# Kernel tuning notes

Measured on AMD Instinct MI355X. Metric: run time of the kernel, lower is better.

Reference implementation:

```python
import jax, jax.numpy as jnp
import numpy as np

B, S, D, H = 4, 2048, 1024, 16
DEPTH = D // H
NEG = 1e10


def setup_inputs() -> dict:
    key = jax.random.key(0)
    ks = jax.random.split(key, 11)
    sc = 0.02
    return {
        "q": jax.random.normal(ks[0], (B, S, D), jnp.float32),
        "v": jax.random.normal(ks[1], (B, S, D), jnp.float32),
        "k": jax.random.normal(ks[2], (B, S, D), jnp.float32),
        "Wq": jax.random.normal(ks[3], (D, D), jnp.float32) * sc,
        "bq": jnp.zeros((D,), jnp.float32),
        "Wk": jax.random.normal(ks[4], (D, D), jnp.float32) * sc,
        "bk": jnp.zeros((D,), jnp.float32),
        "Wv": jax.random.normal(ks[5], (D, D), jnp.float32) * sc,
        "bv": jnp.zeros((D,), jnp.float32),
        "Wo": jax.random.normal(ks[6], (D, D), jnp.float32) * sc,
        "bo": jnp.zeros((D,), jnp.float32),
        "mask": 1,
    }


def _split_heads(x):
    # [B, S, D] -> [B, H, S, depth]
    b, s, _ = x.shape
    return x.reshape(b, s, H, DEPTH).transpose(0, 2, 1, 3)


def reference(q, v, k, Wq, bq, Wk, bk, Wv, bv, Wo, bo, mask):
    qh = _split_heads(q @ Wq + bq)
    kh = _split_heads(k @ Wk + bk)
    vh = _split_heads(v @ Wv + bv)

    scale = 1.0 / jnp.sqrt(jnp.asarray(DEPTH, jnp.float32))
    # [B, H, Sq, Sk]
    logits = jnp.einsum("bhqd,bhkd->bhqk", qh, kh) * scale

    if mask:
        nd, ns = logits.shape[-2], logits.shape[-1]
        i = jnp.arange(nd)[:, None]
        j = jnp.arange(ns)[None, :]
        b = (i >= j - ns + nd).astype(logits.dtype)  # lower triangle from lower-right
        logits = logits * b - NEG * (1.0 - b)

    attn = jax.nn.softmax(logits, axis=-1)
    out = jnp.einsum("bhqk,bhkd->bhqd", attn, vh)  # [B, H, Sq, depth]
    out = out.transpose(0, 2, 1, 3).reshape(q.shape[0], -1, D)  # concat heads
    return out @ Wo + bo
```

## Files before the change

kernel.cpp:

```cpp
#include <hip/hip_runtime.h>
#include <hip/hip_bf16.h>
#include <cstdint>
#include <cstddef>

#define S_LEN 2048
#define D_MODEL 1024
#define N_HEADS 16
#define DEPTH 64
#define BATCH 4

typedef __attribute__((ext_vector_type(4))) float f32x4;
typedef __attribute__((ext_vector_type(8))) short bf16x8;
typedef __attribute__((ext_vector_type(4))) unsigned short us4;
typedef __attribute__((ext_vector_type(8))) unsigned short us8;

__device__ __forceinline__ unsigned short f2bf(float f) {
  unsigned int u = __builtin_bit_cast(unsigned int, f);
  u += 0x7FFFu + ((u >> 16) & 1u);
  return (unsigned short)(u >> 16);
}

__device__ __forceinline__ unsigned short f2bf_hw(float f) {
  return __builtin_bit_cast(unsigned short, __float2bfloat16(f));
}

struct TCArgs {
  const float* W[4];
  unsigned short* Wt[4];
  float scale[4];
};

__global__ __launch_bounds__(256) void transpose_cast4(TCArgs a, int N) {
  __shared__ float tile[32][33];
  int z = blockIdx.z;
  const float* W = a.W[z];
  unsigned short* Wt = a.Wt[z];
  float scale = a.scale[z];
  int bx = blockIdx.x * 32;
  int by = blockIdx.y * 32;
  int tx = threadIdx.x, ty = threadIdx.y;
#pragma unroll
  for (int i = 0; i < 4; ++i)
    tile[ty + i * 8][tx] = W[(size_t)(by + ty + i * 8) * N + bx + tx];
  __syncthreads();
#pragma unroll
  for (int i = 0; i < 4; ++i)
    Wt[(size_t)(bx + ty + i * 8) * N + by + tx] = f2bf(tile[tx][ty + i * 8] * scale);
}

__global__ __launch_bounds__(256) void transpose_v(const unsigned short* __restrict__ Vp,
                                                   unsigned short* __restrict__ Vt) {
  __shared__ unsigned short tile[64][72];
  int tid = threadIdx.x;
  int sb = blockIdx.x;
  int bh = blockIdx.y;
  int b = bh >> 4, h = bh & 15;
  int s0 = sb * 64;
#pragma unroll
  for (int rep = 0; rep < 2; ++rep) {
    int idx = rep * 256 + tid;
    int r = idx >> 3, c8 = idx & 7;
    us8 v = *(const us8*)(Vp + (size_t)(b * S_LEN + s0 + r) * D_MODEL + h * DEPTH + c8 * 8);
#pragma unroll
    for (int e = 0; e < 8; ++e) tile[c8 * 8 + e][r] = v[e];
  }
  __syncthreads();
#pragma unroll
  for (int rep = 0; rep < 2; ++rep) {
    int idx = rep * 256 + tid;
    int d = idx >> 3, c8 = idx & 7;
    us8 v = *(const us8*)&tile[d][c8 * 8];
    *(us8*)(Vt + ((size_t)(bh * DEPTH + d)) * S_LEN + s0 + c8 * 8) = v;
  }
}

struct GemmSlice {
  const void* A;
  const unsigned short* Bt;
  const float* bias;
  void* C;
  float bscale;
};
struct GemmArgs {
  GemmSlice s[3];
};

template <bool A_IS_F32, bool OUT_F32>
__global__ __launch_bounds__(256) void gemm_bt(GemmArgs args, int M, int N, int K) {
  constexpr int ASTR = A_IS_F32 ? 72 : 76;
  constexpr int BSTR = 76;
  __shared__ unsigned short a_lds[128 * ASTR];
  __shared__ unsigned short b_lds[128 * BSTR];

  int slice = blockIdx.y >> 3;
  int nj = blockIdx.y & 7;
  const GemmSlice& g = args.s[slice];
  const float* Af = (const float*)g.A;
  const unsigned short* Ah = (const unsigned short*)g.A;
  const unsigned short* Bt = g.Bt;

  int tid = threadIdx.x;
  int wave = tid >> 6, lane = tid & 63;
  int l15 = lane & 15, lg = lane >> 4;
  int wm = wave >> 1, wn = wave & 1;

  int row0 = blockIdx.x * 128;
  int col0 = nj * 128;

  f32x4 acc[4][4] = {};
  f32x4 av[8];
  us8 avh[4];
  us8 bv[4];

  int ar = tid >> 4, ac4 = tid & 15;
  int br = tid >> 3, bc8 = tid & 7;

  auto loadA = [&](int k0) {
#pragma unroll
    for (int rep = 0; rep < 8; ++rep)
      av[rep] = *(const f32x4*)(Af + (size_t)(row0 + rep * 16 + ar) * K + k0 + ac4 * 4);
  };
  auto writeA = [&]() {
#pragma unroll
    for (int rep = 0; rep < 8; ++rep) {
      us4 h = {f2bf_hw(av[rep][0]), f2bf_hw(av[rep][1]),
               f2bf_hw(av[rep][2]), f2bf_hw(av[rep][3])};
      *(us4*)&a_lds[(rep * 16 + ar) * 72 + ac4 * 4] = h;
    }
  };
  auto loadAh = [&](int k0) {
#pragma unroll
    for (int rep = 0; rep < 4; ++rep)
      avh[rep] = *(const us8*)(Ah + (size_t)(row0 + rep * 32 + br) * K + k0 + bc8 * 8);
  };
  auto writeAh = [&]() {
#pragma unroll
    for (int rep = 0; rep < 4; ++rep)
      *(us8*)&a_lds[(rep * 32 + br) * 76 + bc8 * 8] = avh[rep];
  };
  auto loadB = [&](int k0) {
#pragma unroll
    for (int rep = 0; rep < 4; ++rep)
      bv[rep] = *(const us8*)(Bt + (size_t)(col0 + rep * 32 + br) * K + k0 + bc8 * 8);
  };
  auto writeB = [&]() {
#pragma unroll
    for (int rep = 0; rep < 4; ++rep)
      *(us8*)&b_lds[(rep * 32 + br) * BSTR + bc8 * 8] = bv[rep];
  };
  auto compute = [&]() {
#pragma unroll
    for (int kk = 0; kk < 2; ++kk) {
      bf16x8 af[4], bfr[4];
#pragma unroll
      for (int ii = 0; ii < 4; ++ii) {
        int row = wm * 64 + ii * 16 + l15;
        af[ii] = *(const bf16x8*)&a_lds[row * ASTR + kk * 32 + lg * 8];
      }
#pragma unroll
      for (int jj = 0; jj < 4; ++jj) {
        int row = wn * 64 + jj * 16 + l15;
        bfr[jj] = *(const bf16x8*)&b_lds[row * BSTR + kk * 32 + lg * 8];
      }
#pragma unroll
      for (int ii = 0; ii < 4; ++ii)
#pragma unroll
        for (int jj = 0; jj < 4; ++jj)
          acc[ii][jj] = __builtin_amdgcn_mfma_f32_16x16x32_bf16(af[ii], bfr[jj], acc[ii][jj], 0, 0, 0);
    }
  };

  int nk = K >> 6;
  loadB(0);
  if constexpr (A_IS_F32) loadA(0); else loadAh(0);

  for (int ki = 0; ki < nk; ++ki) {
    __syncthreads();
    writeB();
    if constexpr (A_IS_F32) writeA(); else writeAh();
    __syncthreads();
    if (ki + 1 < nk) {
      loadB((ki + 1) * 64);
      if constexpr (A_IS_F32) loadA((ki + 1) * 64); else loadAh((ki + 1) * 64);
    }
    compute();
  }

#pragma unroll
  for (int ii = 0; ii < 4; ++ii) {
#pragma unroll
    for (int jj = 0; jj < 4; ++jj) {
      int col = col0 + wn * 64 + jj * 16 + l15;
      float bv2 = g.bias[col] * g.bscale;
#pragma unroll
      for (int r = 0; r < 4; ++r) {
        int row = row0 + wm * 64 + ii * 16 + lg * 4 + r;
        float v = acc[ii][jj][r] + bv2;
        if constexpr (OUT_F32)
          ((float*)g.C)[(size_t)row * N + col] = v;
        else
          ((unsigned short*)g.C)[(size_t)row * N + col] = f2bf(v);
      }
    }
  }
}

__global__ __launch_bounds__(256) void attn_kernel(const unsigned short* __restrict__ Qp,
                                                   const unsigned short* __restrict__ Kp,
                                                   const unsigned short* __restrict__ Vt,
                                                   unsigned short* __restrict__ Op) {
  __shared__ unsigned short k_lds[64][76];
  __shared__ unsigned short vt_lds[64][76];
  __shared__ unsigned short p_lds[4][32][76];

  int tid = threadIdx.x;
  int w = tid >> 6, lane = tid & 63;
  int l15 = lane & 15, lg = lane >> 4;

  int bid = blockIdx.x;
  int swz = (bid & 7) * 64 + (bid >> 3);
  int pairIdx = swz & 7;
  int bh = swz >> 3;
  int b = bh >> 4, h = bh & 15;

  const unsigned short* Kbase = Kp + (size_t)b * S_LEN * D_MODEL + h * DEPTH;
  const unsigned short* Vbase = Vt + (size_t)bh * DEPTH * S_LEN;

  bool stageV = (tid >= 128);
  int st = tid & 127;
  int r = st >> 1, cb = (st & 1) * 32;
  const unsigned short* srow = stageV ? (Vbase + (size_t)r * S_LEN + cb)
                                      : (Kbase + (size_t)r * D_MODEL + cb);
  const size_t sstep = stageV ? 64 : (size_t)64 * D_MODEL;

  bf16x8 ones;
#pragma unroll
  for (int e = 0; e < 8; ++e) ones[e] = (short)0x3F80;

  for (int half = 0; half < 2; ++half) {
    int t = (half == 0) ? pairIdx : (15 - pairIdx);
    int q0 = t * 128;
    int nkv = 2 * t + 2;
    int qa0 = q0 + w * 32;

    const unsigned short* qp =
        Qp + ((size_t)(b * S_LEN + qa0 + l15)) * D_MODEL + h * DEPTH;
    bf16x8 qa_0 = *(const bf16x8*)(qp + lg * 8);
    bf16x8 qa_1 = *(const bf16x8*)(qp + 32 + lg * 8);
    bf16x8 qb_0 = *(const bf16x8*)(qp + 16 * D_MODEL + lg * 8);
    bf16x8 qb_1 = *(const bf16x8*)(qp + 16 * D_MODEL + 32 + lg * 8);

    f32x4 acc_la = (f32x4){0.f, 0.f, 0.f, 0.f};
    f32x4 acc_lb = (f32x4){0.f, 0.f, 0.f, 0.f};
    f32x4 acc_oa[4], acc_ob[4];
#pragma unroll
    for (int dd = 0; dd < 4; ++dd) {
      acc_oa[dd] = (f32x4){0.f, 0.f, 0.f, 0.f};
      acc_ob[dd] = (f32x4){0.f, 0.f, 0.f, 0.f};
    }

    const unsigned short* sptr = srow;
    us8 s0 = *(const us8*)sptr;
    us8 s1 = *(const us8*)(sptr + 8);
    us8 s2 = *(const us8*)(sptr + 16);
    us8 s3 = *(const us8*)(sptr + 24);
    sptr += sstep;

    for (int kb = 0; kb < nkv; ++kb) {
      int k0 = kb * 64;
      __syncthreads();
      if (stageV) {
        *(us8*)&vt_lds[r][cb] = s0;
        *(us8*)&vt_lds[r][cb + 8] = s1;
        *(us8*)&vt_lds[r][cb + 16] = s2;
        *(us8*)&vt_lds[r][cb + 24] = s3;
      } else {
        *(us8*)&k_lds[r][cb] = s0;
        *(us8*)&k_lds[r][cb + 8] = s1;
        *(us8*)&k_lds[r][cb + 16] = s2;
        *(us8*)&k_lds[r][cb + 24] = s3;
      }
      __syncthreads();
      bool more = (kb + 1) < nkv;
      if (more) {
        s0 = *(const us8*)sptr;
        s1 = *(const us8*)(sptr + 8);
        s2 = *(const us8*)(sptr + 16);
        s3 = *(const us8*)(sptr + 24);
        sptr += sstep;
      }

      bool doA = k0 <= qa0 + 15;
      bool doB = k0 <= qa0 + 31;
      if (doB) {
        f32x4 sa[4], sb[4];
#pragma unroll
        for (int nf = 0; nf < 4; ++nf) {
          sa[nf] = (f32x4){0.f, 0.f, 0.f, 0.f};
          sb[nf] = (f32x4){0.f, 0.f, 0.f, 0.f};
        }
        __builtin_amdgcn_s_setprio(1);
#pragma unroll
        for (int nf = 0; nf < 4; ++nf) {
          bf16x8 kf0 = *(const bf16x8*)&k_lds[nf * 16 + l15][lg * 8];
          bf16x8 kf1 = *(const bf16x8*)&k_lds[nf * 16 + l15][32 + lg * 8];
          sb[nf] = __builtin_amdgcn_mfma_f32_16x16x32_bf16(qb_0, kf0, sb[nf], 0, 0, 0);
          sb[nf] = __builtin_amdgcn_mfma_f32_16x16x32_bf16(qb_1, kf1, sb[nf], 0, 0, 0);
          if (doA) {
            sa[nf] = __builtin_amdgcn_mfma_f32_16x16x32_bf16(qa_0, kf0, sa[nf], 0, 0, 0);
            sa[nf] = __builtin_amdgcn_mfma_f32_16x16x32_bf16(qa_1, kf1, sa[nf], 0, 0, 0);
          }
        }
        __builtin_amdgcn_s_setprio(0);

        bool diagB = (k0 + 63 > qa0 + 16);
        if (diagB) {
#pragma unroll
          for (int nf = 0; nf < 4; ++nf)
#pragma unroll
            for (int rr = 0; rr < 4; ++rr) {
              int qrow = qa0 + 16 + lg * 4 + rr;
              int kcol = k0 + nf * 16 + l15;
              float x = (kcol > qrow) ? -1e10f : sb[nf][rr];
              float p = __builtin_amdgcn_exp2f(x);
              p_lds[w][16 + lg * 4 + rr][nf * 16 + l15] =
                  (unsigned short)(__builtin_bit_cast(unsigned int, p) >> 16);
            }
        } else {
#pragma unroll
          for (int nf = 0; nf < 4; ++nf)
#pragma unroll
            for (int rr = 0; rr < 4; ++rr) {
              float p = __builtin_amdgcn_exp2f(sb[nf][rr]);
              p_lds[w][16 + lg * 4 + rr][nf * 16 + l15] =
                  (unsigned short)(__builtin_bit_cast(unsigned int, p) >> 16);
            }
        }
        if (doA) {
          bool diagA = (k0 + 63 > qa0);
          if (diagA) {
#pragma unroll
            for (int nf = 0; nf < 4; ++nf)
#pragma unroll
              for (int rr = 0; rr < 4; ++rr) {
                int qrow = qa0 + lg * 4 + rr;
                int kcol = k0 + nf * 16 + l15;
                float x = (kcol > qrow) ? -1e10f : sa[nf][rr];
                float p = __builtin_amdgcn_exp2f(x);
                p_lds[w][lg * 4 + rr][nf * 16 + l15] =
                    (unsigned short)(__builtin_bit_cast(unsigned int, p) >> 16);
              }
          } else {
#pragma unroll
            for (int nf = 0; nf < 4; ++nf)
#pragma unroll
              for (int rr = 0; rr < 4; ++rr) {
                float p = __builtin_amdgcn_exp2f(sa[nf][rr]);
                p_lds[w][lg * 4 + rr][nf * 16 + l15] =
                    (unsigned short)(__builtin_bit_cast(unsigned int, p) >> 16);
              }
          }
        }

        __builtin_amdgcn_s_setprio(1);
#pragma unroll
        for (int kk = 0; kk < 2; ++kk) {
          bf16x8 vf[4];
#pragma unroll
          for (int dd = 0; dd < 4; ++dd)
            vf[dd] = *(const bf16x8*)&vt_lds[dd * 16 + l15][kk * 32 + lg * 8];
          bf16x8 pfb = *(const bf16x8*)&p_lds[w][16 + l15][kk * 32 + lg * 8];
          acc_lb = __builtin_amdgcn_mfma_f32_16x16x32_bf16(pfb, ones, acc_lb, 0, 0, 0);
#pragma unroll
          for (int dd = 0; dd < 4; ++dd)
            acc_ob[dd] = __builtin_amdgcn_mfma_f32_16x16x32_bf16(pfb, vf[dd], acc_ob[dd], 0, 0, 0);
          if (doA) {
            bf16x8 pfa = *(const bf16x8*)&p_lds[w][l15][kk * 32 + lg * 8];
            acc_la = __builtin_amdgcn_mfma_f32_16x16x32_bf16(pfa, ones, acc_la, 0, 0, 0);
#pragma unroll
            for (int dd = 0; dd < 4; ++dd)
              acc_oa[dd] = __builtin_amdgcn_mfma_f32_16x16x32_bf16(pfa, vf[dd], acc_oa[dd], 0, 0, 0);
          }
        }
        __builtin_amdgcn_s_setprio(0);
      }
    }

#pragma unroll
    for (int rr = 0; rr < 4; ++rr) {
      float inva = 1.0f / acc_la[rr];
      float invb = 1.0f / acc_lb[rr];
      int qrowa = qa0 + lg * 4 + rr;
      unsigned short* opa = Op + ((size_t)(b * S_LEN + qrowa)) * D_MODEL + h * DEPTH;
      unsigned short* opb = opa + (size_t)16 * D_MODEL;
#pragma unroll
      for (int dd = 0; dd < 4; ++dd) {
        opa[dd * 16 + l15] = f2bf(acc_oa[dd][rr] * inva);
        opb[dd * 16 + l15] = f2bf(acc_ob[dd][rr] * invb);
      }
    }
  }
}

extern "C" void kernel_launch(void* const* d_in, const int* in_sizes, int n_in,
                              void* d_out, int out_size, void* d_ws, size_t ws_size,
                              hipStream_t stream) {
  const float* q  = (const float*)d_in[0];
  const float* v  = (const float*)d_in[1];
  const float* k  = (const float*)d_in[2];
  const float* Wq = (const float*)d_in[3];
  const float* bq = (const float*)d_in[4];
  const float* Wk = (const float*)d_in[5];
  const float* bk = (const float*)d_in[6];
  const float* Wv = (const float*)d_in[7];
  const float* bv = (const float*)d_in[8];
  const float* Wo = (const float*)d_in[9];
  const float* bo = (const float*)d_in[10];

  char* ws = (char*)d_ws;
  const size_t WSZ = (size_t)D_MODEL * D_MODEL * 2;
  const size_t XSZ = (size_t)BATCH * S_LEN * D_MODEL * 2;
  unsigned short* Wqt = (unsigned short*)(ws);
  unsigned short* Wkt = (unsigned short*)(ws + WSZ);
  unsigned short* Wvt = (unsigned short*)(ws + 2 * WSZ);
  unsigned short* Wot = (unsigned short*)(ws + 3 * WSZ);
  unsigned short* Qp  = (unsigned short*)(ws + 4 * WSZ);
  unsigned short* Kp  = (unsigned short*)(ws + 4 * WSZ + XSZ);
  unsigned short* Vp  = (unsigned short*)(ws + 4 * WSZ + 2 * XSZ);
  unsigned short* Vtp = (unsigned short*)(ws + 4 * WSZ + 3 * XSZ);
  unsigned short* AO  = Vp;

  const float SCL = 0.125f * 1.4426950408889634f;
  const int M = BATCH * S_LEN;

  TCArgs tc{};
  tc.W[0] = Wq;  tc.Wt[0] = Wqt;  tc.scale[0] = SCL;
  tc.W[1] = Wk;  tc.Wt[1] = Wkt;  tc.scale[1] = 1.0f;
  tc.W[2] = Wv;  tc.Wt[2] = Wvt;  tc.scale[2] = 1.0f;
  tc.W[3] = Wo;  tc.Wt[3] = Wot;  tc.scale[3] = 1.0f;
  hipLaunchKernelGGL(transpose_cast4, dim3(D_MODEL / 32, D_MODEL / 32, 4), dim3(32, 8),
                     0, stream, tc, D_MODEL);

  GemmArgs qkv{};
  qkv.s[0] = GemmSlice{(const void*)q, Wqt, bq, (void*)Qp, SCL};
  qkv.s[1] = GemmSlice{(const void*)k, Wkt, bk, (void*)Kp, 1.0f};
  qkv.s[2] = GemmSlice{(const void*)v, Wvt, bv, (void*)Vp, 1.0f};
  hipLaunchKernelGGL((gemm_bt<true, false>), dim3(M / 128, 24), dim3(256), 0, stream,
                     qkv, M, D_MODEL, D_MODEL);

  hipLaunchKernelGGL(transpose_v, dim3(S_LEN / 64, BATCH * N_HEADS), dim3(256), 0, stream,
                     Vp, Vtp);

  hipLaunchKernelGGL(attn_kernel, dim3(512), dim3(256), 0, stream, Qp, Kp, Vtp, AO);

  GemmArgs ao{};
  ao.s[0] = GemmSlice{(const void*)AO, Wot, bo, d_out, 1.0f};
  hipLaunchKernelGGL((gemm_bt<false, true>), dim3(M / 128, 8), dim3(256), 0, stream,
                     ao, M, D_MODEL, D_MODEL);
}
```

Before: 186.3 us.

## Split attention into per-tile blocks and load bf16 GEMM A via direct-to-LDS

The attention kernel now launches one block per 128-row query tile (1024 blocks) instead of pairing a short and a long causal tile in each block. Tiles are ordered in four groups so that long and short tiles are spread across the launch. The aim is more parallelism and shorter per-block tails, at the cost of more blocks and load imbalance left to the hardware scheduler. Separately, the output-projection GEMM loads its bf16 A operand with global_load_lds into an XOR-swizzled, unpadded LDS layout, skipping the register round trip and avoiding bank conflicts.

```diff
diff --git a/kernel.cpp b/kernel.cpp
--- a/kernel.cpp
+++ b/kernel.cpp
@@ -8,6 +8,9 @@
 #define N_HEADS 16
 #define DEPTH 64
 #define BATCH 4
+
+#define GLOBAL_AS __attribute__((address_space(1)))
+#define LDS_AS __attribute__((address_space(3)))
 
 typedef __attribute__((ext_vector_type(4))) float f32x4;
 typedef __attribute__((ext_vector_type(8))) short bf16x8;
@@ -87,10 +90,9 @@
 
 template <bool A_IS_F32, bool OUT_F32>
 __global__ __launch_bounds__(256) void gemm_bt(GemmArgs args, int M, int N, int K) {
-  constexpr int ASTR = A_IS_F32 ? 72 : 76;
-  constexpr int BSTR = 76;
+  constexpr int ASTR = A_IS_F32 ? 72 : 64;
   __shared__ unsigned short a_lds[128 * ASTR];
-  __shared__ unsigned short b_lds[128 * BSTR];
+  __shared__ unsigned short b_lds[128 * 72];
 
   int slice = blockIdx.y >> 3;
   int nj = blockIdx.y & 7;
@@ -109,7 +111,6 @@
 
   f32x4 acc[4][4] = {};
   f32x4 av[8];
-  us8 avh[4];
   us8 bv[4];
 
   int ar = tid >> 4, ac4 = tid & 15;
@@ -128,16 +129,6 @@
       *(us4*)&a_lds[(rep * 16 + ar) * 72 + ac4 * 4] = h;
     }
   };
-  auto loadAh = [&](int k0) {
-#pragma unroll
-    for (int rep = 0; rep < 4; ++rep)
-      avh[rep] = *(const us8*)(Ah + (size_t)(row0 + rep * 32 + br) * K + k0 + bc8 * 8);
-  };
-  auto writeAh = [&]() {
-#pragma unroll
-    for (int rep = 0; rep < 4; ++rep)
-      *(us8*)&a_lds[(rep * 32 + br) * 76 + bc8 * 8] = avh[rep];
-  };
   auto loadB = [&](int k0) {
 #pragma unroll
     for (int rep = 0; rep < 4; ++rep)
@@ -146,7 +137,18 @@
   auto writeB = [&]() {
 #pragma unroll
     for (int rep = 0; rep < 4; ++rep)
-      *(us8*)&b_lds[(rep * 32 + br) * BSTR + bc8 * 8] = bv[rep];
+      *(us8*)&b_lds[(rep * 32 + br) * 72 + bc8 * 8] = bv[rep];
+  };
+  auto issueA = [&](int k0) {
+#pragma unroll
+    for (int rep = 0; rep < 4; ++rep) {
+      int chunk = (wave * 4 + rep) * 64 + lane;
+      int row = chunk >> 3;
+      int c8 = (chunk & 7) ^ (row & 7);
+      __builtin_amdgcn_global_load_lds(
+          (const GLOBAL_AS void*)(Ah + (size_t)(row0 + row) * K + k0 + c8 * 8),
+          (LDS_AS void*)(&a_lds[chunk * 8]), 16, 0, 0);
+    }
   };
   auto compute = [&]() {
 #pragma unroll
@@ -155,12 +157,15 @@
 #pragma unroll
       for (int ii = 0; ii < 4; ++ii) {
         int row = wm * 64 + ii * 16 + l15;
-        af[ii] = *(const bf16x8*)&a_lds[row * ASTR + kk * 32 + lg * 8];
+        if constexpr (A_IS_F32)
+          af[ii] = *(const bf16x8*)&a_lds[row * 72 + kk * 32 + lg * 8];
+        else
+          af[ii] = *(const bf16x8*)&a_lds[row * 64 + (((kk * 4 + lg) ^ (l15 & 7)) * 8)];
       }
 #pragma unroll
       for (int jj = 0; jj < 4; ++jj) {
         int row = wn * 64 + jj * 16 + l15;
-        bfr[jj] = *(const bf16x8*)&b_lds[row * BSTR + kk * 32 + lg * 8];
+        bfr[jj] = *(const bf16x8*)&b_lds[row * 72 + kk * 32 + lg * 8];
       }
 #pragma unroll
       for (int ii = 0; ii < 4; ++ii)
@@ -172,16 +177,19 @@
 
   int nk = K >> 6;
   loadB(0);
-  if constexpr (A_IS_F32) loadA(0); else loadAh(0);
+  if constexpr (A_IS_F32) loadA(0);
 
   for (int ki = 0; ki < nk; ++ki) {
     __syncthreads();
     writeB();
-    if constexpr (A_IS_F32) writeA(); else writeAh();
+    if constexpr (A_IS_F32)
+      writeA();
+    else
+      issueA(ki * 64);
     __syncthreads();
     if (ki + 1 < nk) {
       loadB((ki + 1) * 64);
-      if constexpr (A_IS_F32) loadA((ki + 1) * 64); else loadAh((ki + 1) * 64);
+      if constexpr (A_IS_F32) loadA((ki + 1) * 64);
     }
     compute();
   }
@@ -218,10 +226,14 @@
   int l15 = lane & 15, lg = lane >> 4;
 
   int bid = blockIdx.x;
-  int swz = (bid & 7) * 64 + (bid >> 3);
-  int pairIdx = swz & 7;
-  int bh = swz >> 3;
+  int g = bid >> 8;
+  int rr8 = bid & 255;
+  int bh = rr8 >> 2, j = rr8 & 3;
+  int t = (g == 0) ? j : (g == 1) ? (7 - j) : (g == 2) ? (8 + j) : (15 - j);
   int b = bh >> 4, h = bh & 15;
+
+  int q0 = t * 128;
+  int nkv = 2 * t + 2;
 
   const unsigned short* Kbase = Kp + (size_t)b * S_LEN * D_MODEL + h * DEPTH;
   const unsigned short* Vbase = Vt + (size_t)bh * DEPTH * S_LEN;
@@ -237,93 +249,113 @@
 #pragma unroll
   for (int e = 0; e < 8; ++e) ones[e] = (short)0x3F80;
 
-  for (int half = 0; half < 2; ++half) {
-    int t = (half == 0) ? pairIdx : (15 - pairIdx);
-    int q0 = t * 128;
-    int nkv = 2 * t + 2;
-    int qa0 = q0 + w * 32;
-
-    const unsigned short* qp =
-        Qp + ((size_t)(b * S_LEN + qa0 + l15)) * D_MODEL + h * DEPTH;
-    bf16x8 qa_0 = *(const bf16x8*)(qp + lg * 8);
-    bf16x8 qa_1 = *(const bf16x8*)(qp + 32 + lg * 8);
-    bf16x8 qb_0 = *(const bf16x8*)(qp + 16 * D_MODEL + lg * 8);
-    bf16x8 qb_1 = *(const bf16x8*)(qp + 16 * D_MODEL + 32 + lg * 8);
-
-    f32x4 acc_la = (f32x4){0.f, 0.f, 0.f, 0.f};
-    f32x4 acc_lb = (f32x4){0.f, 0.f, 0.f, 0.f};
-    f32x4 acc_oa[4], acc_ob[4];
-#pragma unroll
-    for (int dd = 0; dd < 4; ++dd) {
-      acc_oa[dd] = (f32x4){0.f, 0.f, 0.f, 0.f};
-      acc_ob[dd] = (f32x4){0.f, 0.f, 0.f, 0.f};
-    }
-
-    const unsigned short* sptr = srow;
-    us8 s0 = *(const us8*)sptr;
-    us8 s1 = *(const us8*)(sptr + 8);
-    us8 s2 = *(const us8*)(sptr + 16);
-    us8 s3 = *(const us8*)(sptr + 24);
-    sptr += sstep;
-
-    for (int kb = 0; kb < nkv; ++kb) {
-      int k0 = kb * 64;
-      __syncthreads();
-      if (stageV) {
-        *(us8*)&vt_lds[r][cb] = s0;
-        *(us8*)&vt_lds[r][cb + 8] = s1;
-        *(us8*)&vt_lds[r][cb + 16] = s2;
-        *(us8*)&vt_lds[r][cb + 24] = s3;
+  int qa0 = q0 + w * 32;
+
+  const unsigned short* qp =
+      Qp + ((size_t)(b * S_LEN + qa0 + l15)) * D_MODEL + h * DEPTH;
+  bf16x8 qa_0 = *(const bf16x8*)(qp + lg * 8);
+  bf16x8 qa_1 = *(const bf16x8*)(qp + 32 + lg * 8);
+  bf16x8 qb_0 = *(const bf16x8*)(qp + 16 * D_MODEL + lg * 8);
+  bf16x8 qb_1 = *(const bf16x8*)(qp + 16 * D_MODEL + 32 + lg * 8);
+
+  f32x4 acc_la = (f32x4){0.f, 0.f, 0.f, 0.f};
+  f32x4 acc_lb = (f32x4){0.f, 0.f, 0.f, 0.f};
+  f32x4 acc_oa[4], acc_ob[4];
+#pragma unroll
+  for (int dd = 0; dd < 4; ++dd) {
+    acc_oa[dd] = (f32x4){0.f, 0.f, 0.f, 0.f};
+    acc_ob[dd] = (f32x4){0.f, 0.f, 0.f, 0.f};
+  }
+
+  const unsigned short* sptr = srow;
+  us8 s0 = *(const us8*)sptr;
+  us8 s1 = *(const us8*)(sptr + 8);
+  us8 s2 = *(const us8*)(sptr + 16);
+  us8 s3 = *(const us8*)(sptr + 24);
+  sptr += sstep;
+
+  for (int kb = 0; kb < nkv; ++kb) {
+    int k0 = kb * 64;
+    __syncthreads();
+    if (stageV) {
+      *(us8*)&vt_lds[r][cb] = s0;
+      *(us8*)&vt_lds[r][cb + 8] = s1;
+      *(us8*)&vt_lds[r][cb + 16] = s2;
+      *(us8*)&vt_lds[r][cb + 24] = s3;
+    } else {
+      *(us8*)&k_lds[r][cb] = s0;
+      *(us8*)&k_lds[r][cb + 8] = s1;
+      *(us8*)&k_lds[r][cb + 16] = s2;
+      *(us8*)&k_lds[r][cb + 24] = s3;
+    }
+    __syncthreads();
+    bool more = (kb + 1) < nkv;
+    if (more) {
+      s0 = *(const us8*)sptr;
+      s1 = *(const us8*)(sptr + 8);
+      s2 = *(const us8*)(sptr + 16);
+      s3 = *(const us8*)(sptr + 24);
+      sptr += sstep;
+    }
+
+    bool doA = k0 <= qa0 + 15;
+    bool doB = k0 <= qa0 + 31;
+    if (doB) {
+      f32x4 sa[4], sb[4];
+#pragma unroll
+      for (int nf = 0; nf < 4; ++nf) {
+        sa[nf] = (f32x4){0.f, 0.f, 0.f, 0.f};
+        sb[nf] = (f32x4){0.f, 0.f, 0.f, 0.f};
+      }
+      __builtin_amdgcn_s_setprio(1);
+#pragma unroll
+      for (int nf = 0; nf < 4; ++nf) {
+        bf16x8 kf0 = *(const bf16x8*)&k_lds[nf * 16 + l15][lg * 8];
+        bf16x8 kf1 = *(const bf16x8*)&k_lds[nf * 16 + l15][32 + lg * 8];
+        sb[nf] = __builtin_amdgcn_mfma_f32_16x16x32_bf16(qb_0, kf0, sb[nf], 0, 0, 0);
+        sb[nf] = __builtin_amdgcn_mfma_f32_16x16x32_bf16(qb_1, kf1, sb[nf], 0, 0, 0);
+        if (doA) {
+          sa[nf] = __builtin_amdgcn_mfma_f32_16x16x32_bf16(qa_0, kf0, sa[nf], 0, 0, 0);
+          sa[nf] = __builtin_amdgcn_mfma_f32_16x16x32_bf16(qa_1, kf1, sa[nf], 0, 0, 0);
+        }
+      }
+      __builtin_amdgcn_s_setprio(0);
+
+      bool diagB = (k0 + 63 > qa0 + 16);
+      if (diagB) {
+#pragma unroll
+        for (int nf = 0; nf < 4; ++nf)
+#pragma unroll
+          for (int rr = 0; rr < 4; ++rr) {
+            int qrow = qa0 + 16 + lg * 4 + rr;
+            int kcol = k0 + nf * 16 + l15;
+            float x = (kcol > qrow) ? -1e10f : sb[nf][rr];
+            float p = __builtin_amdgcn_exp2f(x);
+            p_lds[w][16 + lg * 4 + rr][nf * 16 + l15] =
+                (unsigned short)(__builtin_bit_cast(unsigned int, p) >> 16);
+          }
       } else {
-        *(us8*)&k_lds[r][cb] = s0;
-        *(us8*)&k_lds[r][cb + 8] = s1;
-        *(us8*)&k_lds[r][cb + 16] = s2;
-        *(us8*)&k_lds[r][cb + 24] = s3;
-      }
-      __syncthreads();
-      bool more = (kb + 1) < nkv;
-      if (more) {
-        s0 = *(const us8*)sptr;
-        s1 = *(const us8*)(sptr + 8);
-        s2 = *(const us8*)(sptr + 16);
-        s3 = *(const us8*)(sptr + 24);
-        sptr += sstep;
-      }
-
-      bool doA = k0 <= qa0 + 15;
-      bool doB = k0 <= qa0 + 31;
-      if (doB) {
-        f32x4 sa[4], sb[4];
-#pragma unroll
-        for (int nf = 0; nf < 4; ++nf) {
-          sa[nf] = (f32x4){0.f, 0.f, 0.f, 0.f};
-          sb[nf] = (f32x4){0.f, 0.f, 0.f, 0.f};
-        }
-        __builtin_amdgcn_s_setprio(1);
-#pragma unroll
-        for (int nf = 0; nf < 4; ++nf) {
-          bf16x8 kf0 = *(const bf16x8*)&k_lds[nf * 16 + l15][lg * 8];
-          bf16x8 kf1 = *(const bf16x8*)&k_lds[nf * 16 + l15][32 + lg * 8];
-          sb[nf] = __builtin_amdgcn_mfma_f32_16x16x32_bf16(qb_0, kf0, sb[nf], 0, 0, 0);
-          sb[nf] = __builtin_amdgcn_mfma_f32_16x16x32_bf16(qb_1, kf1, sb[nf], 0, 0, 0);
-          if (doA) {
-            sa[nf] = __builtin_amdgcn_mfma_f32_16x16x32_bf16(qa_0, kf0, sa[nf], 0, 0, 0);
-            sa[nf] = __builtin_amdgcn_mfma_f32_16x16x32_bf16(qa_1, kf1, sa[nf], 0, 0, 0);
+#pragma unroll
+        for (int nf = 0; nf < 4; ++nf)
+#pragma unroll
+          for (int rr = 0; rr < 4; ++rr) {
+            float p = __builtin_amdgcn_exp2f(sb[nf][rr]);
+            p_lds[w][16 + lg * 4 + rr][nf * 16 + l15] =
+                (unsigned short)(__builtin_bit_cast(unsigned int, p) >> 16);
           }
-        }
-        __builtin_amdgcn_s_setprio(0);
-
-        bool diagB = (k0 + 63 > qa0 + 16);
-        if (diagB) {
+      }
+      if (doA) {
+        bool diagA = (k0 + 63 > qa0);
+        if (diagA) {
 #pragma unroll
           for (int nf = 0; nf < 4; ++nf)
 #pragma unroll
             for (int rr = 0; rr < 4; ++rr) {
-              int qrow = qa0 + 16 + lg * 4 + rr;
+              int qrow = qa0 + lg * 4 + rr;
               int kcol = k0 + nf * 16 + l15;
-              float x = (kcol > qrow) ? -1e10f : sb[nf][rr];
+              float x = (kcol > qrow) ? -1e10f : sa[nf][rr];
               float p = __builtin_amdgcn_exp2f(x);
-              p_lds[w][16 + lg * 4 + rr][nf * 16 + l15] =
+              p_lds[w][lg * 4 + rr][nf * 16 + l15] =
                   (unsigned short)(__builtin_bit_cast(unsigned int, p) >> 16);
             }
         } else {
@@ -331,73 +363,48 @@
           for (int nf = 0; nf < 4; ++nf)
 #pragma unroll
             for (int rr = 0; rr < 4; ++rr) {
-              float p = __builtin_amdgcn_exp2f(sb[nf][rr]);
-              p_lds[w][16 + lg * 4 + rr][nf * 16 + l15] =
+              float p = __builtin_amdgcn_exp2f(sa[nf][rr]);
+              p_lds[w][lg * 4 + rr][nf * 16 + l15] =
                   (unsigned short)(__builtin_bit_cast(unsigned int, p) >> 16);
             }
         }
+      }
+
+      __builtin_amdgcn_s_setprio(1);
+#pragma unroll
+      for (int kk = 0; kk < 2; ++kk) {
+        bf16x8 vf[4];
+#pragma unroll
+        for (int dd = 0; dd < 4; ++dd)
+          vf[dd] = *(const bf16x8*)&vt_lds[dd * 16 + l15][kk * 32 + lg * 8];
+        bf16x8 pfb = *(const bf16x8*)&p_lds[w][16 + l15][kk * 32 + lg * 8];
+        acc_lb = __builtin_amdgcn_mfma_f32_16x16x32_bf16(pfb, ones, acc_lb, 0, 0, 0);
+#pragma unroll
+        for (int dd = 0; dd < 4; ++dd)
+          acc_ob[dd] = __builtin_amdgcn_mfma_f32_16x16x32_bf16(pfb, vf[dd], acc_ob[dd], 0, 0, 0);
         if (doA) {
-          bool diagA = (k0 + 63 > qa0);
-          if (diagA) {
-#pragma unroll
-            for (int nf = 0; nf < 4; ++nf)
-#pragma unroll
-              for (int rr = 0; rr < 4; ++rr) {
-                int qrow = qa0 + lg * 4 + rr;
-                int kcol = k0 + nf * 16 + l15;
-                float x = (kcol > qrow) ? -1e10f : sa[nf][rr];
-                float p = __builtin_amdgcn_exp2f(x);
-                p_lds[w][lg * 4 + rr][nf * 16 + l15] =
-                    (unsigned short)(__builtin_bit_cast(unsigned int, p) >> 16);
-              }
-          } else {
-#pragma unroll
-            for (int nf = 0; nf < 4; ++nf)
-#pragma unroll
-              for (int rr = 0; rr < 4; ++rr) {
-                float p = __builtin_amdgcn_exp2f(sa[nf][rr]);
-                p_lds[w][lg * 4 + rr][nf * 16 + l15] =
-                    (unsigned short)(__builtin_bit_cast(unsigned int, p) >> 16);
-              }
-          }
+          bf16x8 pfa = *(const bf16x8*)&p_lds[w][l15][kk * 32 + lg * 8];
+          acc_la = __builtin_amdgcn_mfma_f32_16x16x32_bf16(pfa, ones, acc_la, 0, 0, 0);
+#pragma unroll
+          for (int dd = 0; dd < 4; ++dd)
+            acc_oa[dd] = __builtin_amdgcn_mfma_f32_16x16x32_bf16(pfa, vf[dd], acc_oa[dd], 0, 0, 0);
         }
-
-        __builtin_amdgcn_s_setprio(1);
-#pragma unroll
-        for (int kk = 0; kk < 2; ++kk) {
-          bf16x8 vf[4];
-#pragma unroll
-          for (int dd = 0; dd < 4; ++dd)
-            vf[dd] = *(const bf16x8*)&vt_lds[dd * 16 + l15][kk * 32 + lg * 8];
-          bf16x8 pfb = *(const bf16x8*)&p_lds[w][16 + l15][kk * 32 + lg * 8];
-          acc_lb = __builtin_amdgcn_mfma_f32_16x16x32_bf16(pfb, ones, acc_lb, 0, 0, 0);
-#pragma unroll
-          for (int dd = 0; dd < 4; ++dd)
-            acc_ob[dd] = __builtin_amdgcn_mfma_f32_16x16x32_bf16(pfb, vf[dd], acc_ob[dd], 0, 0, 0);
-          if (doA) {
-            bf16x8 pfa = *(const bf16x8*)&p_lds[w][l15][kk * 32 + lg * 8];
-            acc_la = __builtin_amdgcn_mfma_f32_16x16x32_bf16(pfa, ones, acc_la, 0, 0, 0);
-#pragma unroll
-            for (int dd = 0; dd < 4; ++dd)
-              acc_oa[dd] = __builtin_amdgcn_mfma_f32_16x16x32_bf16(pfa, vf[dd], acc_oa[dd], 0, 0, 0);
-          }
-        }
-        __builtin_amdgcn_s_setprio(0);
-      }
-    }
-
-#pragma unroll
-    for (int rr = 0; rr < 4; ++rr) {
-      float inva = 1.0f / acc_la[rr];
-      float invb = 1.0f / acc_lb[rr];
-      int qrowa = qa0 + lg * 4 + rr;
-      unsigned short* opa = Op + ((size_t)(b * S_LEN + qrowa)) * D_MODEL + h * DEPTH;
-      unsigned short* opb = opa + (size_t)16 * D_MODEL;
-#pragma unroll
-      for (int dd = 0; dd < 4; ++dd) {
-        opa[dd * 16 + l15] = f2bf(acc_oa[dd][rr] * inva);
-        opb[dd * 16 + l15] = f2bf(acc_ob[dd][rr] * invb);
-      }
+      }
+      __builtin_amdgcn_s_setprio(0);
+    }
+  }
+
+#pragma unroll
+  for (int rr = 0; rr < 4; ++rr) {
+    float inva = 1.0f / acc_la[rr];
+    float invb = 1.0f / acc_lb[rr];
+    int qrowa = qa0 + lg * 4 + rr;
+    unsigned short* opa = Op + ((size_t)(b * S_LEN + qrowa)) * D_MODEL + h * DEPTH;
+    unsigned short* opb = opa + (size_t)16 * D_MODEL;
+#pragma unroll
+    for (int dd = 0; dd < 4; ++dd) {
+      opa[dd * 16 + l15] = f2bf(acc_oa[dd][rr] * inva);
+      opb[dd * 16 + l15] = f2bf(acc_ob[dd][rr] * invb);
     }
   }
 }
@@ -451,7 +458,7 @@
   hipLaunchKernelGGL(transpose_v, dim3(S_LEN / 64, BATCH * N_HEADS), dim3(256), 0, stream,
                      Vp, Vtp);
 
-  hipLaunchKernelGGL(attn_kernel, dim3(512), dim3(256), 0, stream, Qp, Kp, Vtp, AO);
+  hipLaunchKernelGGL(attn_kernel, dim3(1024), dim3(256), 0, stream, Qp, Kp, Vtp, AO);
 
   GemmArgs ao{};
   ao.s[0] = GemmSlice{(const void*)AO, Wot, bo, d_out, 1.0f};
```

Measured after the change: 198.8 us. 6.7% more time.
